# Optimization experiments

Measured on AMD Instinct MI355X. Metric: run time of the kernel, lower is better.

## Reference

```python
import jax, jax.numpy as jnp
import numpy as np

N_NODE = 8192
N_EDGE = 131072
IN_DIM = 512
ENC1, ENC2, LAT = 256, 128, 64
DEC1, DEC2 = 128, 256


def _xavier(key, shape):
    fan_in, fan_out = shape
    lim = float(np.sqrt(6.0 / (fan_in + fan_out)))
    return jax.random.uniform(key, shape, jnp.float32, -lim, lim)


def setup_inputs() -> dict:
    key = jax.random.key(0)
    ks = jax.random.split(key, 10)
    x = jax.random.normal(ks[0], (N_NODE, IN_DIM), jnp.float32)
    adj_row = jax.random.randint(ks[1], (N_EDGE,), 0, N_NODE, jnp.int32)
    adj_col = jax.random.randint(ks[2], (N_EDGE,), 0, N_NODE, jnp.int32)
    adj_val = jax.random.uniform(ks[3], (N_EDGE,), jnp.float32)
    return {
        "x": x, "adj_row": adj_row, "adj_col": adj_col, "adj_val": adj_val,
        "W1": _xavier(ks[4], (IN_DIM, ENC1)),
        "W2": _xavier(ks[5], (ENC1, ENC2)),
        "W3": _xavier(ks[6], (ENC2, LAT)),
        "W4": _xavier(ks[7], (LAT, DEC1)),
        "W5": _xavier(ks[8], (DEC1, DEC2)),
        "W6": _xavier(ks[9], (DEC2, IN_DIM)),
    }


def _spmm(row, col, val, dense):
    # sparse [N,N] @ dense [N,D] via edge-list gather + segment-sum scatter
    return jax.ops.segment_sum(val[:, None] * dense[col], row, num_segments=N_NODE)


def _gcn_layer(x, row, col, val, W, active):
    support = x @ W
    if active:
        support = jnp.tanh(support)
    return _spmm(row, col, val, support)


def reference(x, adj_row, adj_col, adj_val, W1, W2, W3, W4, W5, W6):
    # GCNEncoder (dropout = identity at inference)
    h = _gcn_layer(x, adj_row, adj_col, adj_val, W1, True)
    h = _gcn_layer(h, adj_row, adj_col, adj_val, W2, True)
    z_x = _gcn_layer(h, adj_row, adj_col, adj_val, W3, False)
    z_adj = jax.nn.sigmoid(z_x @ z_x.T)
    # GCNDecoder
    h = _gcn_layer(z_x, adj_row, adj_col, adj_val, W4, True)
    h = _gcn_layer(h, adj_row, adj_col, adj_val, W5, True)
    x_hat = _gcn_layer(h, adj_row, adj_col, adj_val, W6, True)
    adj_hat = jax.nn.sigmoid(x_hat @ x_hat.T)
    return (z_x, z_adj, x_hat, adj_hat)
```

## Files before the change

kernel.cpp:

```cpp
#include <hip/hip_runtime.h>
#include <hip/hip_bf16.h>
#include <hip/hip_cooperative_groups.h>

#define NN 8192
#define NE 131072

namespace cg = cooperative_groups;

typedef __attribute__((ext_vector_type(8))) short bfrag;
typedef __attribute__((ext_vector_type(4))) float f32x4;

__device__ __forceinline__ float sigmoidf_(float x){ return 1.0f/(1.0f + __expf(-x)); }

__global__ void k_copyf(const float* __restrict__ in, float* __restrict__ out, int n){
  int i = blockIdx.x*blockDim.x + threadIdx.x;
  if (i < n) out[i] = in[i];
}

__global__ void k_split(const float* __restrict__ in, short* __restrict__ hi,
                        short* __restrict__ lo, int n){
  int i = blockIdx.x*blockDim.x + threadIdx.x;
  if (i < n){
    float v = in[i];
    __hip_bfloat16 h = __float2bfloat16(v);
    float hf = __bfloat162float(h);
    __hip_bfloat16 l = __float2bfloat16(v - hf);
    hi[i] = *(short*)&h;
    lo[i] = *(short*)&l;
  }
}

__global__ void k_zero(int* __restrict__ p, int n){
  int i = blockIdx.x*blockDim.x + threadIdx.x;
  if (i < n) p[i] = 0;
}
__global__ void k_hist(const int* __restrict__ sidx, int* __restrict__ counts){
  int e = blockIdx.x*blockDim.x + threadIdx.x;
  if (e < NE) atomicAdd(&counts[sidx[e]], 1);
}
__global__ void k_scan(const int* __restrict__ counts, int* __restrict__ row_start,
                       int* __restrict__ cursor){
  __shared__ int part[1024];
  int t = threadIdx.x;
  int base = t*8;
  int local[8]; int s = 0;
  #pragma unroll
  for (int i=0;i<8;i++){ s += counts[base+i]; local[i] = s; }
  part[t] = s;
  __syncthreads();
  for (int off=1; off<1024; off<<=1){
    int v = (t >= off) ? part[t-off] : 0;
    __syncthreads();
    part[t] += v;
    __syncthreads();
  }
  int excl = (t==0) ? 0 : part[t-1];
  int run = excl;
  #pragma unroll
  for (int i=0;i<8;i++){
    cursor[base+i] = run;
    run = excl + local[i];
    row_start[base+i+1] = run;
  }
  if (t==0) row_start[0] = 0;
}
__global__ void k_scatter(const int* __restrict__ sidx, const int* __restrict__ gidx,
                          const float* __restrict__ val, int* __restrict__ cursor,
                          int* __restrict__ gath_s, float* __restrict__ val_s){
  int e = blockIdx.x*blockDim.x + threadIdx.x;
  if (e < NE){
    int r = sidx[e];
    int pos = atomicAdd(&cursor[r], 1);
    gath_s[pos] = gidx[e];
    val_s[pos] = val[e];
  }
}

__global__ void k_spmm(const int* __restrict__ row_start, const int* __restrict__ gath_s,
                       const float* __restrict__ val_s, const float* __restrict__ S,
                       float* __restrict__ H, int D){
  int r = blockIdx.x;
  int s0 = row_start[r], s1 = row_start[r+1];
  for (int c = threadIdx.x; c < D; c += blockDim.x){
    float acc = 0.f;
    for (int j = s0; j < s1; ++j)
      acc = fmaf(val_s[j], S[(size_t)gath_s[j]*D + c], acc);
    H[(size_t)r*D + c] = acc;
  }
}

template<int ACT>
__global__ __launch_bounds__(256) void k_gemm64(const float* __restrict__ A,
                                                const float* __restrict__ B,
                                                float* __restrict__ C,
                                                int M, int N, int K){
  __shared__ float As[16][65];
  __shared__ float Bs[16][65];
  int bm = blockIdx.x, bn = blockIdx.y;
  int t = threadIdx.x;
  int tx = t & 15, ty = t >> 4;
  const int rA = t >> 2, kvA = t & 3;
  const int krB = t >> 4, nvB = t & 15;
  float acc[4][4] = {};
  for (int k0 = 0; k0 < K; k0 += 16){
    float4 av = *(const float4*)(A + (size_t)(bm*64 + rA)*K + (k0 + kvA*4));
    float4 bv = *(const float4*)(B + (size_t)(k0 + krB)*N + (bn*64 + nvB*4));
    As[kvA*4+0][rA] = av.x; As[kvA*4+1][rA] = av.y;
    As[kvA*4+2][rA] = av.z; As[kvA*4+3][rA] = av.w;
    Bs[krB][nvB*4+0] = bv.x; Bs[krB][nvB*4+1] = bv.y;
    Bs[krB][nvB*4+2] = bv.z; Bs[krB][nvB*4+3] = bv.w;
    __syncthreads();
    #pragma unroll
    for (int k=0;k<16;k++){
      float a[4], b[4];
      #pragma unroll
      for (int i=0;i<4;i++) a[i] = As[k][ty*4+i];
      #pragma unroll
      for (int j=0;j<4;j++) b[j] = Bs[k][tx*4+j];
      #pragma unroll
      for (int i=0;i<4;i++)
        #pragma unroll
        for (int j=0;j<4;j++)
          acc[i][j] = fmaf(a[i], b[j], acc[i][j]);
    }
    __syncthreads();
  }
  #pragma unroll
  for (int i=0;i<4;i++){
    int rowg = bm*64 + ty*4 + i;
    float4 v;
    v.x = acc[i][0]; v.y = acc[i][1]; v.z = acc[i][2]; v.w = acc[i][3];
    if (ACT == 1){
      v.x = tanhf(v.x); v.y = tanhf(v.y); v.z = tanhf(v.z); v.w = tanhf(v.w);
    }
    *(float4*)(C + (size_t)rowg*N + (bn*64 + tx*4)) = v;
  }
}

__global__ __launch_bounds__(256) void k_syrk_mfma_sig(const short* __restrict__ Hi,
                                                       const short* __restrict__ Lo,
                                                       int K, float* __restrict__ out){
  int bm = blockIdx.x, bn = blockIdx.y;
  if (bn > bm) return;
  __shared__ short LA[2][128][40];
  __shared__ short LB[2][128][40];
  int t = threadIdx.x;
  int wid = t >> 6, lane = t & 63;
  int r0 = lane & 15;
  int kg = lane >> 4;
  f32x4 acc[2][8];
  #pragma unroll
  for (int i=0;i<2;i++)
    #pragma unroll
    for (int j=0;j<8;j++) acc[i][j] = (f32x4){0.f,0.f,0.f,0.f};

  int tr = t >> 1, th = t & 1;
  const short* gAh = Hi + (size_t)(bm*128 + tr)*K + th*16;
  const short* gAl = Lo + (size_t)(bm*128 + tr)*K + th*16;
  const short* gBh = Hi + (size_t)(bn*128 + tr)*K + th*16;
  const short* gBl = Lo + (size_t)(bn*128 + tr)*K + th*16;

  for (int k0 = 0; k0 < K; k0 += 32){
    *(int4*)&LA[0][tr][th*16] = *(const int4*)(gAh + k0);
    *(int4*)&LA[0][tr][th*16+8] = *(const int4*)(gAh + k0 + 8);
    *(int4*)&LA[1][tr][th*16] = *(const int4*)(gAl + k0);
    *(int4*)&LA[1][tr][th*16+8] = *(const int4*)(gAl + k0 + 8);
    *(int4*)&LB[0][tr][th*16] = *(const int4*)(gBh + k0);
    *(int4*)&LB[0][tr][th*16+8] = *(const int4*)(gBh + k0 + 8);
    *(int4*)&LB[1][tr][th*16] = *(const int4*)(gBl + k0);
    *(int4*)&LB[1][tr][th*16+8] = *(const int4*)(gBl + k0 + 8);
    __syncthreads();
    int ar0 = wid*32 + r0, ar1 = wid*32 + 16 + r0;
    bfrag ah0 = *(bfrag*)&LA[0][ar0][kg*8];
    bfrag ah1 = *(bfrag*)&LA[0][ar1][kg*8];
    bfrag al0 = *(bfrag*)&LA[1][ar0][kg*8];
    bfrag al1 = *(bfrag*)&LA[1][ar1][kg*8];
    #pragma unroll
    for (int j=0;j<8;j++){
      int bc = j*16 + r0;
      bfrag bh = *(bfrag*)&LB[0][bc][kg*8];
      bfrag bl = *(bfrag*)&LB[1][bc][kg*8];
      acc[0][j] = __builtin_amdgcn_mfma_f32_16x16x32_bf16(ah0, bh, acc[0][j], 0,0,0);
      acc[0][j] = __builtin_amdgcn_mfma_f32_16x16x32_bf16(ah0, bl, acc[0][j], 0,0,0);
      acc[0][j] = __builtin_amdgcn_mfma_f32_16x16x32_bf16(al0, bh, acc[0][j], 0,0,0);
      acc[1][j] = __builtin_amdgcn_mfma_f32_16x16x32_bf16(ah1, bh, acc[1][j], 0,0,0);
      acc[1][j] = __builtin_amdgcn_mfma_f32_16x16x32_bf16(ah1, bl, acc[1][j], 0,0,0);
      acc[1][j] = __builtin_amdgcn_mfma_f32_16x16x32_bf16(al1, bh, acc[1][j], 0,0,0);
    }
    __syncthreads();
  }
  #pragma unroll
  for (int i=0;i<2;i++){
    int rb = bm*128 + wid*32 + i*16 + kg*4;
    #pragma unroll
    for (int j=0;j<8;j++){
      int cb = bn*128 + j*16 + r0;
      #pragma unroll
      for (int v=0;v<4;v++){
        float s = sigmoidf_(acc[i][j][v]);
        out[(size_t)(rb+v)*NN + cb] = s;
        if (bm != bn) out[(size_t)cb*NN + (rb+v)] = s;
      }
    }
  }
}

__global__ __launch_bounds__(256) void k_syrk128_sig(const float* __restrict__ X, int K,
                                                     float* __restrict__ out){
  int bm = blockIdx.x, bn = blockIdx.y;
  if (bn > bm) return;
  __shared__ float As[16][128];
  __shared__ float Bs[16][128];
  int t = threadIdx.x;
  int tx = t & 15, ty = t >> 4;
  int rL = t >> 1, sL = (t & 1) << 3;
  float acc[4][4][4] = {};
  for (int k0 = 0; k0 < K; k0 += 16){
    const float* pa = X + (size_t)(bm*128 + rL)*K + (k0 + sL);
    const float* pb = X + (size_t)(bn*128 + rL)*K + (k0 + sL);
    float4 a0 = *(const float4*)pa, a1 = *(const float4*)(pa+4);
    float4 b0 = *(const float4*)pb, b1 = *(const float4*)(pb+4);
    As[sL+0][rL]=a0.x; As[sL+1][rL]=a0.y; As[sL+2][rL]=a0.z; As[sL+3][rL]=a0.w;
    As[sL+4][rL]=a1.x; As[sL+5][rL]=a1.y; As[sL+6][rL]=a1.z; As[sL+7][rL]=a1.w;
    Bs[sL+0][rL]=b0.x; Bs[sL+1][rL]=b0.y; Bs[sL+2][rL]=b0.z; Bs[sL+3][rL]=b0.w;
    Bs[sL+4][rL]=b1.x; Bs[sL+5][rL]=b1.y; Bs[sL+6][rL]=b1.z; Bs[sL+7][rL]=b1.w;
    __syncthreads();
    #pragma unroll
    for (int k=0;k<16;k++){
      float4 a0v = *(const float4*)&As[k][ty*4];
      float4 a1v = *(const float4*)&As[k][64 + ty*4];
      float4 b0v = *(const float4*)&Bs[k][tx*4];
      float4 b1v = *(const float4*)&Bs[k][64 + tx*4];
      float ar[8] = {a0v.x,a0v.y,a0v.z,a0v.w, a1v.x,a1v.y,a1v.z,a1v.w};
      float br[8] = {b0v.x,b0v.y,b0v.z,b0v.w, b1v.x,b1v.y,b1v.z,b1v.w};
      #pragma unroll
      for (int sub=0; sub<4; ++sub){
        int ai = (sub>>1)<<2, bj = (sub&1)<<2;
        #pragma unroll
        for (int i=0;i<4;i++)
          #pragma unroll
          for (int j=0;j<4;j++)
            acc[sub][i][j] = fmaf(ar[ai+i], br[bj+j], acc[sub][i][j]);
      }
    }
    __syncthreads();
  }
  #pragma unroll
  for (int sub=0; sub<4; ++sub)
    #pragma unroll
    for (int i=0;i<4;i++)
      #pragma unroll
      for (int j=0;j<4;j++)
        acc[sub][i][j] = sigmoidf_(acc[sub][i][j]);
  #pragma unroll
  for (int sub=0; sub<4; ++sub){
    int rb = bm*128 + ((sub>>1)<<6) + ty*4;
    int cb = bn*128 + ((sub&1)<<6) + tx*4;
    #pragma unroll
    for (int i=0;i<4;i++){
      float4 v;
      v.x = acc[sub][i][0]; v.y = acc[sub][i][1];
      v.z = acc[sub][i][2]; v.w = acc[sub][i][3];
      *(float4*)(out + (size_t)(rb+i)*NN + cb) = v;
    }
    if (bm != bn){
      #pragma unroll
      for (int j=0;j<4;j++){
        float4 w;
        w.x = acc[sub][0][j]; w.y = acc[sub][1][j];
        w.z = acc[sub][2][j]; w.w = acc[sub][3][j];
        *(float4*)(out + (size_t)(cb+j)*NN + rb) = w;
      }
    }
  }
}

__global__ __launch_bounds__(256) void k_syrk_sig(const float* __restrict__ X, int K,
                                                  float* __restrict__ out, int bm0){
  __shared__ float As[16][65];
  __shared__ float Bs[16][65];
  int bm = blockIdx.x + bm0, bn = blockIdx.y;
  int t = threadIdx.x;
  int tx = t & 15, ty = t >> 4;
  const int rL = t >> 2, kvL = t & 3;
  float acc[4][4] = {};
  for (int k0 = 0; k0 < K; k0 += 16){
    float4 av = *(const float4*)(X + (size_t)(bm*64 + rL)*K + (k0 + kvL*4));
    float4 bv = *(const float4*)(X + (size_t)(bn*64 + rL)*K + (k0 + kvL*4));
    As[kvL*4+0][rL] = av.x; As[kvL*4+1][rL] = av.y;
    As[kvL*4+2][rL] = av.z; As[kvL*4+3][rL] = av.w;
    Bs[kvL*4+0][rL] = bv.x; Bs[kvL*4+1][rL] = bv.y;
    Bs[kvL*4+2][rL] = bv.z; Bs[kvL*4+3][rL] = bv.w;
    __syncthreads();
    #pragma unroll
    for (int k=0;k<16;k++){
      float a[4], b[4];
      #pragma unroll
      for (int i=0;i<4;i++) a[i] = As[k][ty*4+i];
      #pragma unroll
      for (int j=0;j<4;j++) b[j] = Bs[k][tx*4+j];
      #pragma unroll
      for (int i=0;i<4;i++)
        #pragma unroll
        for (int j=0;j<4;j++)
          acc[i][j] = fmaf(a[i], b[j], acc[i][j]);
    }
    __syncthreads();
  }
  #pragma unroll
  for (int i=0;i<4;i++){
    int rowg = bm*64 + ty*4 + i;
    float4 v;
    v.x = sigmoidf_(acc[i][0]); v.y = sigmoidf_(acc[i][1]);
    v.z = sigmoidf_(acc[i][2]); v.w = sigmoidf_(acc[i][3]);
    *(float4*)(out + (size_t)rowg*NN + (bn*64 + tx*4)) = v;
  }
}

__global__ __launch_bounds__(256) void k_zcoop(const float* __restrict__ Z,
                                               float* __restrict__ zadj){
  __shared__ float Za[64][65];
  __shared__ float Zb[64][65];
  int bm = blockIdx.x;
  int bn = blockIdx.y;
  int t = threadIdx.x;
  #pragma unroll
  for (int q=0;q<4;q++){
    int lin = q*256 + t;
    int r  = lin >> 4;
    int kq = lin & 15;
    float4 a = *(const float4*)(Z + (size_t)(bm*64 + r)*64 + kq*4);
    float4 b = *(const float4*)(Z + (size_t)(bn*64 + r)*64 + kq*4);
    Za[kq*4+0][r] = a.x; Za[kq*4+1][r] = a.y; Za[kq*4+2][r] = a.z; Za[kq*4+3][r] = a.w;
    Zb[kq*4+0][r] = b.x; Zb[kq*4+1][r] = b.y; Zb[kq*4+2][r] = b.z; Zb[kq*4+3][r] = b.w;
  }
  cg::this_grid().sync();
  int tx = t & 15, ty = t >> 4;
  float acc[4][4] = {};
  #pragma unroll 16
  for (int k=0;k<64;k++){
    float a[4], b[4];
    #pragma unroll
    for (int i=0;i<4;i++) a[i] = Za[k][ty*4+i];
    #pragma unroll
    for (int j=0;j<4;j++) b[j] = Zb[k][tx*4+j];
    #pragma unroll
    for (int i=0;i<4;i++)
      #pragma unroll
      for (int j=0;j<4;j++)
        acc[i][j] = fmaf(a[i], b[j], acc[i][j]);
  }
  #pragma unroll
  for (int i=0;i<4;i++){
    int rowg = bm*64 + ty*4 + i;
    float4 v;
    v.x = sigmoidf_(acc[i][0]); v.y = sigmoidf_(acc[i][1]);
    v.z = sigmoidf_(acc[i][2]); v.w = sigmoidf_(acc[i][3]);
    *(float4*)(zadj + (size_t)rowg*NN + (bn*64 + tx*4)) = v;
  }
}

extern "C" void kernel_launch(void* const* d_in, const int* in_sizes, int n_in,
                              void* d_out, int out_size, void* d_ws, size_t ws_size,
                              hipStream_t stream){
  (void)in_sizes; (void)n_in; (void)out_size;
  const float* x       = (const float*)d_in[0];
  const int*   adj_row = (const int*)d_in[1];
  const int*   adj_col = (const int*)d_in[2];
  const float* adj_val = (const float*)d_in[3];
  const float* W1 = (const float*)d_in[4];
  const float* W2 = (const float*)d_in[5];
  const float* W3 = (const float*)d_in[6];
  const float* W4 = (const float*)d_in[7];
  const float* W5 = (const float*)d_in[8];
  const float* W6 = (const float*)d_in[9];

  float* out      = (float*)d_out;
  float* zx_out   = out;
  float* zadj_out = out + 524288;
  float* xhat_out = out + 67633152;
  float* adj_out  = out + 71827456;

  const size_t MiB = (size_t)1 << 20;
  char* R1 = (char*)zadj_out;
  float* Z   = (float*)(R1 + 0*MiB);
  float* S   = (float*)(R1 + 4*MiB);
  float* H   = (float*)(R1 + 24*MiB);
  short* XHi = (short*)(R1 + 34*MiB);
  short* XLo = (short*)(R1 + 43*MiB);
  int*   counts    = (int*)(R1 + 52*MiB);
  int*   row_start = counts + NN;
  int*   cursor    = row_start + NN + 1;
  int*   gath_s    = cursor + NN;
  float* val_s     = (float*)(gath_s + NE);
  float* Zws = (float*)d_ws;
  const bool use_ws = (ws_size >= 2*MiB);

  k_zero<<<NN/256, 256, 0, stream>>>(counts, NN);
  k_hist<<<NE/256, 256, 0, stream>>>(adj_row, counts);
  k_scan<<<1, 1024, 0, stream>>>(counts, row_start, cursor);
  k_scatter<<<NE/256, 256, 0, stream>>>(adj_row, adj_col, adj_val, cursor, gath_s, val_s);

  k_gemm64<1><<<dim3(128,4), 256, 0, stream>>>(x, W1, S, NN, 256, 512);
  k_spmm<<<NN, 256, 0, stream>>>(row_start, gath_s, val_s, S, H, 256);
  k_gemm64<1><<<dim3(128,2), 256, 0, stream>>>(H, W2, S, NN, 128, 256);
  k_spmm<<<NN, 128, 0, stream>>>(row_start, gath_s, val_s, S, H, 128);
  k_gemm64<0><<<dim3(128,1), 256, 0, stream>>>(H, W3, S, NN, 64, 128);
  k_spmm<<<NN, 64, 0, stream>>>(row_start, gath_s, val_s, S, Z, 64);
  if (use_ws) k_copyf<<<2048, 256, 0, stream>>>(Z, Zws, NN*64);
  k_copyf<<<2048, 256, 0, stream>>>(Z, zx_out, NN*64);

  k_gemm64<1><<<dim3(128,2), 256, 0, stream>>>(Z, W4, S, NN, 128, 64);
  k_spmm<<<NN, 128, 0, stream>>>(row_start, gath_s, val_s, S, H, 128);
  k_gemm64<1><<<dim3(128,4), 256, 0, stream>>>(H, W5, S, NN, 256, 128);
  k_spmm<<<NN, 256, 0, stream>>>(row_start, gath_s, val_s, S, H, 256);
  k_gemm64<1><<<dim3(128,8), 256, 0, stream>>>(H, W6, S, NN, 512, 256);
  k_spmm<<<NN, 256, 0, stream>>>(row_start, gath_s, val_s, S, xhat_out, 512);

  k_split<<<16384, 256, 0, stream>>>(xhat_out, XHi, XLo, NN*512);
  k_syrk_mfma_sig<<<dim3(64,64), 256, 0, stream>>>(XHi, XLo, 512, adj_out);

  if (use_ws){
    k_syrk128_sig<<<dim3(64,64), 256, 0, stream>>>(Zws, 64, zadj_out);
  } else {
    k_syrk_sig<<<dim3(127,128), 256, 0, stream>>>(Z, 64, zadj_out, 1);
    const float* Zp = Z; float* zp = zadj_out;
    void* args[] = { (void*)&Zp, (void*)&zp };
    hipLaunchCooperativeKernel((const void*)k_zcoop, dim3(1,128), dim3(256,1,1),
                               args, 0, stream);
  }
}
```

Measured before the change: 710.0 us.

## Use 128x128 register-tiled GEMM and fuse bf16 split into final SpMM

Adds a 128x128-tile FP32 GEMM in which each thread computes an 8x8 output block, and uses it for five of the six dense layers. This raises arithmetic intensity and cuts shared-memory traffic per FMA, but halves the grid (64-128 blocks on a 256-CU part) and raises register pressure. It also folds the hi/lo bf16 split of x_hat into the last SpMM kernel. That removes a separate pass that re-read 16 MB of x_hat.

```diff
diff --git a/kernel.cpp b/kernel.cpp
--- a/kernel.cpp
+++ b/kernel.cpp
@@ -15,19 +15,6 @@
 __global__ void k_copyf(const float* __restrict__ in, float* __restrict__ out, int n){
   int i = blockIdx.x*blockDim.x + threadIdx.x;
   if (i < n) out[i] = in[i];
-}
-
-__global__ void k_split(const float* __restrict__ in, short* __restrict__ hi,
-                        short* __restrict__ lo, int n){
-  int i = blockIdx.x*blockDim.x + threadIdx.x;
-  if (i < n){
-    float v = in[i];
-    __hip_bfloat16 h = __float2bfloat16(v);
-    float hf = __bfloat162float(h);
-    __hip_bfloat16 l = __float2bfloat16(v - hf);
-    hi[i] = *(short*)&h;
-    lo[i] = *(short*)&l;
-  }
 }
 
 __global__ void k_zero(int* __restrict__ p, int n){
@@ -86,6 +73,26 @@
     for (int j = s0; j < s1; ++j)
       acc = fmaf(val_s[j], S[(size_t)gath_s[j]*D + c], acc);
     H[(size_t)r*D + c] = acc;
+  }
+}
+
+__global__ void k_spmm_split(const int* __restrict__ row_start, const int* __restrict__ gath_s,
+                             const float* __restrict__ val_s, const float* __restrict__ S,
+                             float* __restrict__ H, short* __restrict__ hi,
+                             short* __restrict__ lo, int D){
+  int r = blockIdx.x;
+  int s0 = row_start[r], s1 = row_start[r+1];
+  for (int c = threadIdx.x; c < D; c += blockDim.x){
+    float acc = 0.f;
+    for (int j = s0; j < s1; ++j)
+      acc = fmaf(val_s[j], S[(size_t)gath_s[j]*D + c], acc);
+    size_t idx = (size_t)r*D + c;
+    H[idx] = acc;
+    __hip_bfloat16 h = __float2bfloat16(acc);
+    float hf = __bfloat162float(h);
+    __hip_bfloat16 l = __float2bfloat16(acc - hf);
+    hi[idx] = *(short*)&h;
+    lo[idx] = *(short*)&l;
   }
 }
 
@@ -134,6 +141,66 @@
       v.x = tanhf(v.x); v.y = tanhf(v.y); v.z = tanhf(v.z); v.w = tanhf(v.w);
     }
     *(float4*)(C + (size_t)rowg*N + (bn*64 + tx*4)) = v;
+  }
+}
+
+template<int ACT>
+__global__ __launch_bounds__(256) void k_gemm128(const float* __restrict__ A,
+                                                 const float* __restrict__ B,
+                                                 float* __restrict__ C,
+                                                 int M, int N, int K){
+  __shared__ float As[16][128];
+  __shared__ float Bs[16][128];
+  int bm = blockIdx.x, bn = blockIdx.y;
+  int t = threadIdx.x;
+  int tx = t & 15, ty = t >> 4;
+  int rL = t >> 1, sL = (t & 1) << 3;
+  int krB = t >> 4, cqB = (t & 15) << 3;
+  float acc[4][4][4] = {};
+  for (int k0 = 0; k0 < K; k0 += 16){
+    const float* pa = A + (size_t)(bm*128 + rL)*K + (k0 + sL);
+    float4 a0 = *(const float4*)pa, a1 = *(const float4*)(pa+4);
+    As[sL+0][rL]=a0.x; As[sL+1][rL]=a0.y; As[sL+2][rL]=a0.z; As[sL+3][rL]=a0.w;
+    As[sL+4][rL]=a1.x; As[sL+5][rL]=a1.y; As[sL+6][rL]=a1.z; As[sL+7][rL]=a1.w;
+    const float* pb = B + (size_t)(k0 + krB)*N + bn*128 + cqB;
+    float4 b0 = *(const float4*)pb, b1 = *(const float4*)(pb+4);
+    *(float4*)&Bs[krB][cqB]   = b0;
+    *(float4*)&Bs[krB][cqB+4] = b1;
+    __syncthreads();
+    #pragma unroll
+    for (int k=0;k<16;k++){
+      float4 a0v = *(const float4*)&As[k][ty*4];
+      float4 a1v = *(const float4*)&As[k][64 + ty*4];
+      float4 b0v = *(const float4*)&Bs[k][tx*4];
+      float4 b1v = *(const float4*)&Bs[k][64 + tx*4];
+      float ar[8] = {a0v.x,a0v.y,a0v.z,a0v.w, a1v.x,a1v.y,a1v.z,a1v.w};
+      float br[8] = {b0v.x,b0v.y,b0v.z,b0v.w, b1v.x,b1v.y,b1v.z,b1v.w};
+      #pragma unroll
+      for (int sub=0; sub<4; ++sub){
+        int ai = (sub>>1)<<2, bj = (sub&1)<<2;
+        #pragma unroll
+        for (int i=0;i<4;i++)
+          #pragma unroll
+          for (int j=0;j<4;j++)
+            acc[sub][i][j] = fmaf(ar[ai+i], br[bj+j], acc[sub][i][j]);
+      }
+    }
+    __syncthreads();
+  }
+  #pragma unroll
+  for (int sub=0; sub<4; ++sub){
+    int rb = bm*128 + ((sub>>1)<<6) + ty*4;
+    int cb = bn*128 + ((sub&1)<<6) + tx*4;
+    #pragma unroll
+    for (int i=0;i<4;i++){
+      float4 v;
+      v.x = acc[sub][i][0]; v.y = acc[sub][i][1];
+      v.z = acc[sub][i][2]; v.w = acc[sub][i][3];
+      if (ACT == 1){
+        v.x = tanhf(v.x); v.y = tanhf(v.y); v.z = tanhf(v.z); v.w = tanhf(v.w);
+      }
+      *(float4*)(C + (size_t)(rb+i)*N + cb) = v;
+    }
   }
 }
 
@@ -401,23 +468,23 @@
   k_scan<<<1, 1024, 0, stream>>>(counts, row_start, cursor);
   k_scatter<<<NE/256, 256, 0, stream>>>(adj_row, adj_col, adj_val, cursor, gath_s, val_s);
 
-  k_gemm64<1><<<dim3(128,4), 256, 0, stream>>>(x, W1, S, NN, 256, 512);
+  k_gemm128<1><<<dim3(64,2), 256, 0, stream>>>(x, W1, S, NN, 256, 512);
   k_spmm<<<NN, 256, 0, stream>>>(row_start, gath_s, val_s, S, H, 256);
-  k_gemm64<1><<<dim3(128,2), 256, 0, stream>>>(H, W2, S, NN, 128, 256);
+  k_gemm128<1><<<dim3(64,1), 256, 0, stream>>>(H, W2, S, NN, 128, 256);
   k_spmm<<<NN, 128, 0, stream>>>(row_start, gath_s, val_s, S, H, 128);
   k_gemm64<0><<<dim3(128,1), 256, 0, stream>>>(H, W3, S, NN, 64, 128);
   k_spmm<<<NN, 64, 0, stream>>>(row_start, gath_s, val_s, S, Z, 64);
   if (use_ws) k_copyf<<<2048, 256, 0, stream>>>(Z, Zws, NN*64);
   k_copyf<<<2048, 256, 0, stream>>>(Z, zx_out, NN*64);
 
-  k_gemm64<1><<<dim3(128,2), 256, 0, stream>>>(Z, W4, S, NN, 128, 64);
+  k_gemm128<1><<<dim3(64,1), 256, 0, stream>>>(Z, W4, S, NN, 128, 64);
   k_spmm<<<NN, 128, 0, stream>>>(row_start, gath_s, val_s, S, H, 128);
-  k_gemm64<1><<<dim3(128,4), 256, 0, stream>>>(H, W5, S, NN, 256, 128);
+  k_gemm128<1><<<dim3(64,2), 256, 0, stream>>>(H, W5, S, NN, 256, 128);
   k_spmm<<<NN, 256, 0, stream>>>(row_start, gath_s, val_s, S, H, 256);
-  k_gemm64<1><<<dim3(128,8), 256, 0, stream>>>(H, W6, S, NN, 512, 256);
-  k_spmm<<<NN, 256, 0, stream>>>(row_start, gath_s, val_s, S, xhat_out, 512);
-
-  k_split<<<16384, 256, 0, stream>>>(xhat_out, XHi, XLo, NN*512);
+  k_gemm128<1><<<dim3(64,4), 256, 0, stream>>>(H, W6, S, NN, 512, 256);
+  k_spmm_split<<<NN, 256, 0, stream>>>(row_start, gath_s, val_s, S, xhat_out,
+                                       XHi, XLo, 512);
+
   k_syrk_mfma_sig<<<dim3(64,64), 256, 0, stream>>>(XHi, XLo, 512, adj_out);
 
   if (use_ws){
```

Measured after the change: 746.7 us. 1.05x slower.
